# Optimization experiments

Hardware: AMD Instinct MI355X
Metric: run time of the kernel (lower is better)

## Reference

```python
import jax, jax.numpy as jnp
import numpy as np

N = 4096          # num_nodes
U = 2048          # num_users
R = 5             # num_relations
B = 30            # num_bases
H0 = 500          # hidden_size[0]
H1 = 75           # hidden_size[1]
E = 262144        # num_edges
EPS = 1e-5


def setup_inputs() -> dict:
    key = jax.random.key(0)
    ks = jax.random.split(key, 10)
    x = jax.random.normal(ks[0], (N, N), dtype=jnp.float32)
    edge_index = jax.random.randint(ks[1], (2, E), 0, N, dtype=jnp.int64)
    edge_type = jax.random.randint(ks[2], (E,), 0, R, dtype=jnp.int64)
    # RGCNConv basis-decomposition parameters
    basis = jax.random.normal(ks[3], (B, N, H0), dtype=jnp.float32) * 0.02
    comp = jax.random.normal(ks[4], (R, B), dtype=jnp.float32) * 0.1
    root = jax.random.normal(ks[5], (N, H0), dtype=jnp.float32) * 0.02
    bias_rgcn = jnp.zeros((H0,), dtype=jnp.float32)
    # DenseLayer (Linear without bias) + BatchNorm1d affine params
    fc_w = jax.random.normal(ks[6], (H1, H0), dtype=jnp.float32) * 0.05
    bn_gamma_u = jnp.ones((U,), dtype=jnp.float32)
    bn_beta_u = jnp.zeros((U,), dtype=jnp.float32)
    bn_gamma_i = jnp.ones((N - U,), dtype=jnp.float32)
    bn_beta_i = jnp.zeros((N - U,), dtype=jnp.float32)
    return {
        "x": x, "basis": basis, "comp": comp, "root": root,
        "bias_rgcn": bias_rgcn, "fc_w": fc_w,
        "bn_gamma_u": bn_gamma_u, "bn_beta_u": bn_beta_u,
        "bn_gamma_i": bn_gamma_i, "bn_beta_i": bn_beta_i,
        "edge_index": edge_index, "edge_type": edge_type,
    }


def _bn1d(z, gamma, beta):
    # BatchNorm1d applied to z.unsqueeze(0): channels = rows, normalize over feature dim
    mu = z.mean(axis=1, keepdims=True)
    var = ((z - mu) ** 2).mean(axis=1, keepdims=True)
    return gamma[:, None] * (z - mu) / jnp.sqrt(var + EPS) + beta[:, None]


def _forward(x, basis, comp, root, bias_rgcn, fc_w,
             bn_gamma_u, bn_beta_u, bn_gamma_i, bn_beta_i,
             edge_index, edge_type):
    # --- RGCNConv with basis decomposition, mean aggregation per relation ---
    W = jnp.einsum('rb,bio->rio', comp, basis)          # [R, N, H0]
    h = jnp.einsum('ni,rio->rno', x, W)                 # [R, N, H0] transformed feats
    src, dst = edge_index[0], edge_index[1]
    msgs = h[edge_type, src]                            # [E, H0] gather
    seg = dst * R + edge_type                           # (target, relation) segments
    sums = jax.ops.segment_sum(msgs, seg, num_segments=N * R)
    cnt = jax.ops.segment_sum(jnp.ones((E,), dtype=msgs.dtype), seg, num_segments=N * R)
    agg = (sums / jnp.maximum(cnt, 1.0)[:, None]).reshape(N, R, H0).sum(axis=1)
    feats = agg + x @ root + bias_rgcn                  # [N, H0]

    # --- separate (accum != 'stack') ---
    u, i = feats[:U], feats[U:]

    # --- DenseLayer: dropout (eval: identity) -> Linear(no bias) -> BN -> ReLU ---
    u = jax.nn.relu(_bn1d(u @ fc_w.T, bn_gamma_u, bn_beta_u))
    i = jax.nn.relu(_bn1d(i @ fc_w.T, bn_gamma_i, bn_beta_i))
    return u, i


def reference(x, basis, comp, root, bias_rgcn, fc_w,
              bn_gamma_u, bn_beta_u, bn_gamma_i, bn_beta_i,
              edge_index, edge_type):
    return _forward(x, basis, comp, root, bias_rgcn, fc_w,
                    bn_gamma_u, bn_beta_u, bn_gamma_i, bn_beta_i,
                    edge_index, edge_type)
```

## Files before the change

kernel.cpp:

```cpp
#include <hip/hip_runtime.h>
#include <hip/hip_bf16.h>
#include <stdint.h>

#define N_NODES 4096
#define U_NODES 2048
#define R_REL 5
#define B_BASES 30
#define H0 500
#define H1 75
#define E_EDGES 262144
#define EPS_BN 1e-5f
#define K_DIM 4096
#define M_COLS 3000
#define M_PAD 3072
#define NSEG (N_NODES*R_REL)

typedef __attribute__((ext_vector_type(4))) float f32x4;
typedef __attribute__((ext_vector_type(8))) short bf16x8;

static __device__ __forceinline__ ushort bf16_bits(float f) {
    union { float f; uint32_t u; } c; c.f = f;
    uint32_t u = c.u;
    uint32_t r = (u + 0x7fffu + ((u >> 16) & 1u)) >> 16;
    return (ushort)r;
}

static __device__ __forceinline__ void async_copy16(const ushort* g, ushort* l) {
    __builtin_amdgcn_global_load_lds((const __attribute__((address_space(1))) void*)g,
                                     (__attribute__((address_space(3))) void*)l,
                                     16, 0, 0);
}

__global__ void k_convert_x(const float* __restrict__ x, ushort* __restrict__ xb) {
    int i = (blockIdx.x * 256 + threadIdx.x) * 4;
    float4 v = *(const float4*)(x + i);
    ushort4 o;
    o.x = bf16_bits(v.x); o.y = bf16_bits(v.y);
    o.z = bf16_bits(v.z); o.w = bf16_bits(v.w);
    *(ushort4*)(xb + i) = o;
}

__global__ void k_make_wallT(const float* __restrict__ basis, const float* __restrict__ comp,
                             const float* __restrict__ root, ushort* __restrict__ wallT) {
    __shared__ float compl_[R_REL * B_BASES];
    __shared__ float T[32][33];
    int t = threadIdx.x;
    if (t < R_REL * B_BASES) compl_[t] = comp[t];
    __syncthreads();
    int k0 = blockIdx.x * 32, o0 = blockIdx.y * 32;
    int o_in = t & 31, k_in = t >> 5;
    int o = o0 + o_in;
    bool ov = (o < H0);
    float acc[4][6];
    #pragma unroll
    for (int a = 0; a < 4; a++)
        #pragma unroll
        for (int r = 0; r < 6; r++) acc[a][r] = 0.f;
    for (int b = 0; b < B_BASES; b++) {
        float cw[5];
        #pragma unroll
        for (int r = 0; r < 5; r++) cw[r] = compl_[r * B_BASES + b];
        #pragma unroll
        for (int a = 0; a < 4; a++) {
            int k = k0 + a * 8 + k_in;
            float v = ov ? basis[(size_t)b * K_DIM * H0 + (size_t)k * H0 + o] : 0.f;
            #pragma unroll
            for (int r = 0; r < 5; r++) acc[a][r] += cw[r] * v;
        }
    }
    #pragma unroll
    for (int a = 0; a < 4; a++) {
        int k = k0 + a * 8 + k_in;
        acc[a][5] = ov ? root[(size_t)k * H0 + o] : 0.f;
    }
    for (int r = 0; r < 6; r++) {
        __syncthreads();
        #pragma unroll
        for (int a = 0; a < 4; a++) T[o_in][a * 8 + k_in] = acc[a][r];
        __syncthreads();
        int ro = t >> 5, ck = t & 31;
        #pragma unroll
        for (int a = 0; a < 4; a++) {
            int oo = ro + a * 8;
            int om = o0 + oo;
            if (om < H0) {
                int m = r * H0 + om;
                wallT[(size_t)m * K_DIM + k0 + ck] = bf16_bits(T[oo][ck]);
            }
        }
    }
}

__global__ __launch_bounds__(256) void k_gemm(const ushort* __restrict__ A,
                                              const ushort* __restrict__ BT,
                                              float* __restrict__ C) {
    __shared__ __align__(16) ushort As[128 * 64];
    __shared__ __align__(16) ushort Bs[128 * 64];
    int tid = threadIdx.x;
    int lane = tid & 63, wave = tid >> 6;
    int m0 = blockIdx.x * 128, n0 = blockIdx.y * 128;
    int wm = (wave & 1) * 64, wn = (wave >> 1) * 64;

    f32x4 acc[4][4];
    #pragma unroll
    for (int a = 0; a < 4; a++)
        #pragma unroll
        for (int b = 0; b < 4; b++) { f32x4 z = {0.f, 0.f, 0.f, 0.f}; acc[a][b] = z; }

    int srow = tid >> 3;
    int skc = (((tid & 7) ^ ((tid >> 3) & 7))) * 8;
    const ushort* Abase = A + (size_t)(m0 + srow) * K_DIM + skc;
    const ushort* Bbase = BT + (size_t)(n0 + srow) * K_DIM + skc;
    int ldsoff = (wave * 64) * 8;

    for (int k0 = 0; k0 < K_DIM; k0 += 64) {
        const ushort* ga = Abase + k0;
        const ushort* gb = Bbase + k0;
        #pragma unroll
        for (int i = 0; i < 4; i++) {
            async_copy16(ga + (size_t)i * 32 * K_DIM, As + i * 2048 + ldsoff);
            async_copy16(gb + (size_t)i * 32 * K_DIM, Bs + i * 2048 + ldsoff);
        }
        __syncthreads();
        #pragma unroll
        for (int kk = 0; kk < 64; kk += 32) {
            bf16x8 af[4], bfr[4];
            int koff = kk + ((lane >> 4) * 8);
            int g = koff >> 3;
            #pragma unroll
            for (int a = 0; a < 4; a++) {
                int row = wm + a * 16 + (lane & 15);
                int sw = (g ^ (row & 7)) * 8;
                af[a] = *(const bf16x8*)(As + row * 64 + sw);
            }
            #pragma unroll
            for (int b = 0; b < 4; b++) {
                int row = wn + b * 16 + (lane & 15);
                int sw = (g ^ (row & 7)) * 8;
                bfr[b] = *(const bf16x8*)(Bs + row * 64 + sw);
            }
            #pragma unroll
            for (int a = 0; a < 4; a++)
                #pragma unroll
                for (int b = 0; b < 4; b++)
                    acc[a][b] = __builtin_amdgcn_mfma_f32_16x16x32_bf16(af[a], bfr[b], acc[a][b], 0, 0, 0);
        }
        __syncthreads();
    }

    int col = lane & 15;
    int rbase = (lane >> 4) * 4;
    #pragma unroll
    for (int a = 0; a < 4; a++) {
        #pragma unroll
        for (int b = 0; b < 4; b++) {
            int gn = n0 + wn + b * 16 + col;
            if (gn < M_COLS) {
                #pragma unroll
                for (int r = 0; r < 4; r++) {
                    int gm = m0 + wm + a * 16 + rbase + r;
                    C[(size_t)gm * M_COLS + gn] = acc[a][b][r];
                }
            }
        }
    }
}

__global__ void k_count(const int* __restrict__ ei, const int* __restrict__ et, int* __restrict__ cnt) {
    int e = blockIdx.x * 256 + threadIdx.x;
    if (e < E_EDGES) {
        int dst = ei[E_EDGES + e];
        int r = et[e];
        atomicAdd(&cnt[dst * R_REL + r], 1);
    }
}

__global__ void k_scan(const int* __restrict__ cnt, int* __restrict__ offs, int* __restrict__ cursor) {
    __shared__ int part[256];
    int t = threadIdx.x;
    const int CH = NSEG / 256;
    int s = 0;
    for (int i = 0; i < CH; i++) s += cnt[t * CH + i];
    part[t] = s;
    __syncthreads();
    for (int d = 1; d < 256; d <<= 1) {
        int v = (t >= d) ? part[t - d] : 0;
        __syncthreads();
        part[t] += v;
        __syncthreads();
    }
    int run = part[t] - s;
    for (int i = 0; i < CH; i++) {
        int idx = t * CH + i;
        offs[idx] = run;
        cursor[idx] = run;
        run += cnt[idx];
    }
    if (t == 255) offs[NSEG] = run;
}

__global__ void k_fill(const int* __restrict__ ei, const int* __restrict__ et,
                       int* __restrict__ cursor, int* __restrict__ edge_src) {
    int e = blockIdx.x * 256 + threadIdx.x;
    if (e < E_EDGES) {
        int src = ei[e];
        int dst = ei[E_EDGES + e];
        int r = et[e];
        int pos = atomicAdd(&cursor[dst * R_REL + r], 1);
        edge_src[pos] = src;
    }
}

__global__ void k_agg(const float* __restrict__ C, const int* __restrict__ offs,
                      const int* __restrict__ edge_src, const float* __restrict__ bias,
                      float* __restrict__ feats) {
    int n = blockIdx.x;
    int t = threadIdx.x;
    if (t >= 125) return;
    f32x4 acc = {0.f, 0.f, 0.f, 0.f};
    #pragma unroll
    for (int r = 0; r < R_REL; r++) {
        int seg = n * R_REL + r;
        int beg = offs[seg], end = offs[seg + 1];
        if (end > beg) {
            f32x4 s = {0.f, 0.f, 0.f, 0.f};
            for (int e = beg; e < end; e++) {
                int src = edge_src[e];
                s += *(const f32x4*)(C + (size_t)src * M_COLS + r * H0 + t * 4);
            }
            float inv = 1.0f / (float)(end - beg);
            acc += s * inv;
        }
    }
    acc += *(const f32x4*)(C + (size_t)n * M_COLS + 5 * H0 + t * 4);
    acc += *(const f32x4*)(bias + t * 4);
    *(f32x4*)(feats + (size_t)n * H0 + t * 4) = acc;
}

__global__ __launch_bounds__(256) void k_fc_bn(const float* __restrict__ feats, const float* __restrict__ fcw,
                                               const float* __restrict__ gu, const float* __restrict__ bu,
                                               const float* __restrict__ gi, const float* __restrict__ bi,
                                               float* __restrict__ out) {
    __shared__ float z[4][80];
    int t = threadIdx.x;
    int lane = t & 63, wave = t >> 6;
    int row = blockIdx.x * 4 + wave;
    float f[8];
    #pragma unroll
    for (int i = 0; i < 8; i++) {
        int k = lane + 64 * i;
        f[i] = (k < H0) ? feats[(size_t)row * H0 + k] : 0.f;
    }
    for (int j = 0; j < H1; j++) {
        float d = 0.f;
        #pragma unroll
        for (int i = 0; i < 8; i++) {
            int k = lane + 64 * i;
            float w = (k < H0) ? fcw[(size_t)j * H0 + k] : 0.f;
            d += f[i] * w;
        }
        #pragma unroll
        for (int s = 32; s > 0; s >>= 1) d += __shfl_xor(d, s);
        if (lane == 0) z[wave][j] = d;
    }
    __syncthreads();
    float a = (lane < H1) ? z[wave][lane] : 0.f;
    float b2 = (lane < H1 - 64) ? z[wave][64 + lane] : 0.f;
    float s1 = a + b2, s2 = a * a + b2 * b2;
    #pragma unroll
    for (int s = 32; s > 0; s >>= 1) { s1 += __shfl_xor(s1, s); s2 += __shfl_xor(s2, s); }
    float mean = s1 / (float)H1;
    float var = s2 / (float)H1 - mean * mean;
    float inv = 1.0f / sqrtf(var + EPS_BN);
    float gamma, beta;
    if (row < U_NODES) { gamma = gu[row];            beta = bu[row]; }
    else               { gamma = gi[row - U_NODES];  beta = bi[row - U_NODES]; }
    if (lane < H1) {
        float v = gamma * (a - mean) * inv + beta;
        out[(size_t)row * H1 + lane] = v > 0.f ? v : 0.f;
    }
    if (lane < H1 - 64) {
        float v = gamma * (b2 - mean) * inv + beta;
        out[(size_t)row * H1 + 64 + lane] = v > 0.f ? v : 0.f;
    }
}

extern "C" void kernel_launch(void* const* d_in, const int* in_sizes, int n_in,
                              void* d_out, int out_size, void* d_ws, size_t ws_size,
                              hipStream_t stream) {
    (void)in_sizes; (void)n_in; (void)out_size; (void)ws_size;
    const float* x         = (const float*)d_in[0];
    const float* basis     = (const float*)d_in[1];
    const float* comp      = (const float*)d_in[2];
    const float* root      = (const float*)d_in[3];
    const float* bias_rgcn = (const float*)d_in[4];
    const float* fc_w      = (const float*)d_in[5];
    const float* gu        = (const float*)d_in[6];
    const float* bu        = (const float*)d_in[7];
    const float* gi        = (const float*)d_in[8];
    const float* bi        = (const float*)d_in[9];
    const int*   ei        = (const int*)d_in[10];
    const int*   et        = (const int*)d_in[11];
    float* out = (float*)d_out;

    char* ws = (char*)d_ws;
    size_t off = 0;
    auto carve = [&](size_t bytes) -> void* {
        void* p = ws + off;
        off += (bytes + 255) & ~(size_t)255;
        return p;
    };
    ushort* xb      = (ushort*)carve((size_t)N_NODES * K_DIM * 2);
    ushort* wallT   = (ushort*)carve((size_t)M_PAD * K_DIM * 2);
    float*  hall    = (float*) carve((size_t)N_NODES * M_COLS * 4);
    float*  feats   = (float*) carve((size_t)N_NODES * H0 * 4);
    int*    cnt     = (int*)   carve((size_t)NSEG * 4);
    int*    offs    = (int*)   carve((size_t)(NSEG + 1) * 4);
    int*    cursor  = (int*)   carve((size_t)NSEG * 4);
    int*    edge_src= (int*)   carve((size_t)E_EDGES * 4);

    hipMemsetAsync(cnt, 0, NSEG * 4, stream);
    k_convert_x<<<16384, 256, 0, stream>>>(x, xb);
    k_make_wallT<<<dim3(128, 16), 256, 0, stream>>>(basis, comp, root, wallT);
    k_count<<<E_EDGES / 256, 256, 0, stream>>>(ei, et, cnt);
    k_scan<<<1, 256, 0, stream>>>(cnt, offs, cursor);
    k_fill<<<E_EDGES / 256, 256, 0, stream>>>(ei, et, cursor, edge_src);
    k_gemm<<<dim3(32, 24), 256, 0, stream>>>(xb, wallT, hall);
    k_agg<<<N_NODES, 128, 0, stream>>>(hall, offs, edge_src, bias_rgcn, feats);
    k_fc_bn<<<N_NODES / 4, 256, 0, stream>>>(feats, fc_w, gu, bu, gi, bi, out);
}
```

Baseline: 666.1 us.

## Store GEMM output in bf16 and restructure fc+BN kernel with shared-memory rows

The GEMM now writes its transformed features in bf16 rather than fp32, which halves the intermediate buffer and the bytes the aggregation kernel gathers per edge. The aggregation kernel converts back to fp32 while accumulating. The fc+BN kernel is rewritten so each thread computes one output column for four rows staged in shared memory, replacing per-column wave shuffle reductions. The trade-off is extra rounding error on the intermediate features and a different fc reduction order.

```diff
diff --git a/kernel.cpp b/kernel.cpp
--- a/kernel.cpp
+++ b/kernel.cpp
@@ -25,6 +25,10 @@
     return (ushort)r;
 }
 
+static __device__ __forceinline__ float bf16_to_f(ushort u) {
+    union { uint32_t u; float f; } c; c.u = ((uint32_t)u) << 16; return c.f;
+}
+
 static __device__ __forceinline__ void async_copy16(const ushort* g, ushort* l) {
     __builtin_amdgcn_global_load_lds((const __attribute__((address_space(1))) void*)g,
                                      (__attribute__((address_space(3))) void*)l,
@@ -93,7 +97,7 @@
 
 __global__ __launch_bounds__(256) void k_gemm(const ushort* __restrict__ A,
                                               const ushort* __restrict__ BT,
-                                              float* __restrict__ C) {
+                                              ushort* __restrict__ C) {
     __shared__ __align__(16) ushort As[128 * 64];
     __shared__ __align__(16) ushort Bs[128 * 64];
     int tid = threadIdx.x;
@@ -159,7 +163,7 @@
                 #pragma unroll
                 for (int r = 0; r < 4; r++) {
                     int gm = m0 + wm + a * 16 + rbase + r;
-                    C[(size_t)gm * M_COLS + gn] = acc[a][b][r];
+                    C[(size_t)gm * M_COLS + gn] = bf16_bits(acc[a][b][r]);
                 }
             }
         }
@@ -211,7 +215,7 @@
     }
 }
 
-__global__ void k_agg(const float* __restrict__ C, const int* __restrict__ offs,
+__global__ void k_agg(const ushort* __restrict__ C, const int* __restrict__ offs,
                       const int* __restrict__ edge_src, const float* __restrict__ bias,
                       float* __restrict__ feats) {
     int n = blockIdx.x;
@@ -226,62 +230,74 @@
             f32x4 s = {0.f, 0.f, 0.f, 0.f};
             for (int e = beg; e < end; e++) {
                 int src = edge_src[e];
-                s += *(const f32x4*)(C + (size_t)src * M_COLS + r * H0 + t * 4);
+                ushort4 v = *(const ushort4*)(C + (size_t)src * M_COLS + r * H0 + t * 4);
+                s.x += bf16_to_f(v.x); s.y += bf16_to_f(v.y);
+                s.z += bf16_to_f(v.z); s.w += bf16_to_f(v.w);
             }
             float inv = 1.0f / (float)(end - beg);
             acc += s * inv;
         }
     }
-    acc += *(const f32x4*)(C + (size_t)n * M_COLS + 5 * H0 + t * 4);
+    {
+        ushort4 v = *(const ushort4*)(C + (size_t)n * M_COLS + 5 * H0 + t * 4);
+        acc.x += bf16_to_f(v.x); acc.y += bf16_to_f(v.y);
+        acc.z += bf16_to_f(v.z); acc.w += bf16_to_f(v.w);
+    }
     acc += *(const f32x4*)(bias + t * 4);
     *(f32x4*)(feats + (size_t)n * H0 + t * 4) = acc;
 }
 
-__global__ __launch_bounds__(256) void k_fc_bn(const float* __restrict__ feats, const float* __restrict__ fcw,
+__global__ __launch_bounds__(128) void k_fc_bn(const float* __restrict__ feats, const float* __restrict__ fcw,
                                                const float* __restrict__ gu, const float* __restrict__ bu,
                                                const float* __restrict__ gi, const float* __restrict__ bi,
                                                float* __restrict__ out) {
+    __shared__ float fs[4][H0];
     __shared__ float z[4][80];
     int t = threadIdx.x;
+    int row0 = blockIdx.x * 4;
+    if (t < 125) {
+        #pragma unroll
+        for (int r = 0; r < 4; r++)
+            *(f32x4*)&fs[r][t * 4] = *(const f32x4*)(feats + (size_t)(row0 + r) * H0 + t * 4);
+    }
+    __syncthreads();
+    if (t < H1) {
+        float a0 = 0.f, a1 = 0.f, a2 = 0.f, a3 = 0.f;
+        const float* wr = fcw + (size_t)t * H0;
+        for (int k = 0; k < H0; k += 4) {
+            float4 w = *(const float4*)(wr + k);
+            a0 += w.x * fs[0][k] + w.y * fs[0][k+1] + w.z * fs[0][k+2] + w.w * fs[0][k+3];
+            a1 += w.x * fs[1][k] + w.y * fs[1][k+1] + w.z * fs[1][k+2] + w.w * fs[1][k+3];
+            a2 += w.x * fs[2][k] + w.y * fs[2][k+1] + w.z * fs[2][k+2] + w.w * fs[2][k+3];
+            a3 += w.x * fs[3][k] + w.y * fs[3][k+1] + w.z * fs[3][k+2] + w.w * fs[3][k+3];
+        }
+        z[0][t] = a0; z[1][t] = a1; z[2][t] = a2; z[3][t] = a3;
+    }
+    __syncthreads();
     int lane = t & 63, wave = t >> 6;
-    int row = blockIdx.x * 4 + wave;
-    float f[8];
-    #pragma unroll
-    for (int i = 0; i < 8; i++) {
-        int k = lane + 64 * i;
-        f[i] = (k < H0) ? feats[(size_t)row * H0 + k] : 0.f;
-    }
-    for (int j = 0; j < H1; j++) {
-        float d = 0.f;
-        #pragma unroll
-        for (int i = 0; i < 8; i++) {
-            int k = lane + 64 * i;
-            float w = (k < H0) ? fcw[(size_t)j * H0 + k] : 0.f;
-            d += f[i] * w;
-        }
-        #pragma unroll
-        for (int s = 32; s > 0; s >>= 1) d += __shfl_xor(d, s);
-        if (lane == 0) z[wave][j] = d;
-    }
-    __syncthreads();
-    float a = (lane < H1) ? z[wave][lane] : 0.f;
-    float b2 = (lane < H1 - 64) ? z[wave][64 + lane] : 0.f;
-    float s1 = a + b2, s2 = a * a + b2 * b2;
-    #pragma unroll
-    for (int s = 32; s > 0; s >>= 1) { s1 += __shfl_xor(s1, s); s2 += __shfl_xor(s2, s); }
-    float mean = s1 / (float)H1;
-    float var = s2 / (float)H1 - mean * mean;
-    float inv = 1.0f / sqrtf(var + EPS_BN);
-    float gamma, beta;
-    if (row < U_NODES) { gamma = gu[row];            beta = bu[row]; }
-    else               { gamma = gi[row - U_NODES];  beta = bi[row - U_NODES]; }
-    if (lane < H1) {
-        float v = gamma * (a - mean) * inv + beta;
-        out[(size_t)row * H1 + lane] = v > 0.f ? v : 0.f;
-    }
-    if (lane < H1 - 64) {
-        float v = gamma * (b2 - mean) * inv + beta;
-        out[(size_t)row * H1 + 64 + lane] = v > 0.f ? v : 0.f;
+    #pragma unroll
+    for (int rr = 0; rr < 2; rr++) {
+        int r = wave * 2 + rr;
+        int row = row0 + r;
+        float a = (lane < H1) ? z[r][lane] : 0.f;
+        float b2 = (lane < H1 - 64) ? z[r][64 + lane] : 0.f;
+        float s1 = a + b2, s2 = a * a + b2 * b2;
+        #pragma unroll
+        for (int s = 32; s > 0; s >>= 1) { s1 += __shfl_xor(s1, s); s2 += __shfl_xor(s2, s); }
+        float mean = s1 / (float)H1;
+        float var = s2 / (float)H1 - mean * mean;
+        float inv = 1.0f / sqrtf(var + EPS_BN);
+        float gamma, beta;
+        if (row < U_NODES) { gamma = gu[row];            beta = bu[row]; }
+        else               { gamma = gi[row - U_NODES];  beta = bi[row - U_NODES]; }
+        if (lane < H1) {
+            float v = gamma * (a - mean) * inv + beta;
+            out[(size_t)row * H1 + lane] = v > 0.f ? v : 0.f;
+        }
+        if (lane < H1 - 64) {
+            float v = gamma * (b2 - mean) * inv + beta;
+            out[(size_t)row * H1 + 64 + lane] = v > 0.f ? v : 0.f;
+        }
     }
 }
 
@@ -312,7 +328,7 @@
     };
     ushort* xb      = (ushort*)carve((size_t)N_NODES * K_DIM * 2);
     ushort* wallT   = (ushort*)carve((size_t)M_PAD * K_DIM * 2);
-    float*  hall    = (float*) carve((size_t)N_NODES * M_COLS * 4);
+    ushort* hall    = (ushort*)carve((size_t)N_NODES * M_COLS * 2);
     float*  feats   = (float*) carve((size_t)N_NODES * H0 * 4);
     int*    cnt     = (int*)   carve((size_t)NSEG * 4);
     int*    offs    = (int*)   carve((size_t)(NSEG + 1) * 4);
@@ -327,5 +343,5 @@
     k_fill<<<E_EDGES / 256, 256, 0, stream>>>(ei, et, cursor, edge_src);
     k_gemm<<<dim3(32, 24), 256, 0, stream>>>(xb, wallT, hall);
     k_agg<<<N_NODES, 128, 0, stream>>>(hall, offs, edge_src, bias_rgcn, feats);
-    k_fc_bn<<<N_NODES / 4, 256, 0, stream>>>(feats, fc_w, gu, bu, gi, bi, out);
-}
+    k_fc_bn<<<N_NODES / 4, 128, 0, stream>>>(feats, fc_w, gu, bu, gi, bi, out);
+}
```

Result: faster. 627.1 us (-5.9%).
